# Optimization experiments

Hardware: AMD Instinct MI355X
Metric: run time of the kernel (lower is better)

Reference implementation:

```python
import jax, jax.numpy as jnp
import numpy as np

D, L, H = 256, 8, 64  # data_dim, latent_dim, hidden_dim (depth=3 hidden layers)


def setup_inputs() -> dict:
    key = jax.random.key(0)
    ks = jax.random.split(key, 9)
    s_in = 1.0 / np.sqrt(L)
    s_h = 1.0 / np.sqrt(H)
    return {
        "z": jax.random.normal(ks[0], (4096, D, L), dtype=jnp.float32),
        # stacked per-coordinate MLP params: layer i weight (D, in, out), bias (D, out)
        "W1": jax.random.uniform(ks[1], (D, L, H), jnp.float32, -s_in, s_in),
        "b1": jax.random.uniform(ks[2], (D, H), jnp.float32, -s_in, s_in),
        "W2": jax.random.uniform(ks[3], (D, H, H), jnp.float32, -s_h, s_h),
        "b2": jax.random.uniform(ks[4], (D, H), jnp.float32, -s_h, s_h),
        "W3": jax.random.uniform(ks[5], (D, H, H), jnp.float32, -s_h, s_h),
        "b3": jax.random.uniform(ks[6], (D, H), jnp.float32, -s_h, s_h),
        "Wo": jax.random.uniform(ks[7], (D, H, 1), jnp.float32, -s_h, s_h),
        "bo": jax.random.uniform(ks[8], (D, 1), jnp.float32, -s_h, s_h),
    }


def reference(z, W1, b1, W2, b2, W3, b3, Wo, bo):
    # Batched grouped MLP: all data_dim per-coordinate nets in one einsum per layer.
    h = jax.nn.silu(jnp.einsum("bdl,dlh->bdh", z, W1) + b1)   # (B, D, H)
    h = jax.nn.silu(jnp.einsum("bdh,dhk->bdk", h, W2) + b2)
    h = jax.nn.silu(jnp.einsum("bdh,dhk->bdk", h, W3) + b3)
    out = jnp.einsum("bdh,dho->bdo", h, Wo) + bo              # (B, D, 1)
    return out[..., 0]                                        # (B, D) == torch.cat(coords, dim=1)
```

## Files before the change

kernel.cpp:

```cpp
#include <hip/hip_runtime.h>
#include <hip/hip_bf16.h>


#define NDIM 256
#define LDIM 8
#define HDIM 64
#define BDIM 4096
#define BT   128

#define REC_W1P   0
#define REC_W2H   3072
#define REC_W2L   11264
#define REC_W3H   19456
#define REC_W3L   27648
#define REC_COEF  35840
#define REC_SIZE  36864

#define ACT_HI    0
#define OUTBUF    16384
#define LDS_SIZE  17408

typedef __bf16 bf16x8 __attribute__((ext_vector_type(8)));
typedef __bf16 bf16x4 __attribute__((ext_vector_type(4)));
typedef float  f32x4  __attribute__((ext_vector_type(4)));

__device__ __forceinline__ float silu_f(float x) {
  return x * __builtin_amdgcn_rcpf(1.0f + __expf(-x));
}

__global__ void setup_weights(const float* __restrict__ W1, const float* __restrict__ b1,
                              const float* __restrict__ W2, const float* __restrict__ b2,
                              const float* __restrict__ W3, const float* __restrict__ b3,
                              const float* __restrict__ Wo, char* __restrict__ ws) {
  const int d = blockIdx.x;
  const int y = blockIdx.y;
  const int t = threadIdx.x;
  __shared__ float tile[64 * 65];
  char* rec = ws + (size_t)d * REC_SIZE;

  if (y == 0) {
    for (int idx = t; idx < LDIM * HDIM; idx += 256)
      tile[(idx >> 6) * 65 + (idx & 63)] = W1[d * LDIM * HDIM + idx];
    __syncthreads();
    if (t < 64) {
      __bf16* w1p = (__bf16*)(rec + REC_W1P) + t * 24;
#pragma unroll
      for (int ks = 0; ks < 8; ++ks) {
        float f = tile[ks * 65 + t];
        __bf16 h = (__bf16)f;
        w1p[ks] = h;
        w1p[8 + ks] = h;
        w1p[16 + ks] = (__bf16)(f - (float)h);
      }
    }
    float* coef = (float*)(rec + REC_COEF);
    float v;
    if (t < 64)       v = b1[d * 64 + t];
    else if (t < 128) v = b2[d * 64 + (t - 64)];
    else if (t < 192) v = b3[d * 64 + (t - 128)];
    else              v = Wo[d * 64 + (t - 192)];
    coef[t] = v;
  } else {
    const float* src = (y == 1 ? W2 : W3) + (size_t)d * 4096;
    const int hibase = (y == 1 ? REC_W2H : REC_W3H);
    for (int idx = t; idx < 4096; idx += 256)
      tile[(idx >> 6) * 65 + (idx & 63)] = src[idx];
    __syncthreads();
    const int o = t >> 2;
    const int q = t & 3;
    bf16x8 h0, h1, l0, l1;
#pragma unroll
    for (int j = 0; j < 8; ++j) {
      float f = tile[(q * 16 + j) * 65 + o];
      __bf16 h = (__bf16)f;
      h0[j] = h; l0[j] = (__bf16)(f - (float)h);
      float g = tile[(q * 16 + 8 + j) * 65 + o];
      __bf16 hg = (__bf16)g;
      h1[j] = hg; l1[j] = (__bf16)(g - (float)hg);
    }
    char* dst = rec + hibase + o * 128 + q * 32;
    *(bf16x8*)(dst)              = h0;
    *(bf16x8*)(dst + 16)         = h1;
    *(bf16x8*)(dst + 8192)       = l0;
    *(bf16x8*)(dst + 8192 + 16)  = l1;
  }
}

__device__ __forceinline__ void mid_layer(const char* __restrict__ wh, const float* __restrict__ biasf,
                                          const char* __restrict__ smem, f32x4 (&acc)[2][4],
                                          int wm, int wp, int l15, int lg, int x7) {
  const int co = (lg ^ x7) * 16;
#pragma unroll
  for (int mt = 0; mt < 2; ++mt) {
    f32x4 b = *(const f32x4*)(biasf + wm * 32 + mt * 16 + lg * 4);
#pragma unroll
    for (int nt = 0; nt < 4; ++nt) acc[mt][nt] = b;
  }
  const char* aw[2];
  int ab[4];
#pragma unroll
  for (int mt = 0; mt < 2; ++mt) aw[mt] = wh + (wm * 32 + mt * 16 + l15) * 128 + lg * 16;
#pragma unroll
  for (int nt = 0; nt < 4; ++nt) ab[nt] = ACT_HI + (wp * 64 + nt * 16 + l15) * 128 + co;

#pragma unroll
  for (int ks = 0; ks < 2; ++ks) {
    const int kx = ks * 64;
    bf16x8 ah[2], al[2], bh[4];
#pragma unroll
    for (int mt = 0; mt < 2; ++mt) {
      const char* p = aw[mt] + kx;
      ah[mt] = *(const bf16x8*)p;
      al[mt] = *(const bf16x8*)(p + 8192);
    }
#pragma unroll
    for (int nt = 0; nt < 4; ++nt)
      bh[nt] = *(const bf16x8*)(smem + (ab[nt] ^ kx));
#pragma unroll
    for (int mt = 0; mt < 2; ++mt)
#pragma unroll
      for (int nt = 0; nt < 4; ++nt)
        acc[mt][nt] = __builtin_amdgcn_mfma_f32_16x16x32_bf16(ah[mt], bh[nt], acc[mt][nt], 0, 0, 0);
#pragma unroll
    for (int mt = 0; mt < 2; ++mt)
#pragma unroll
      for (int nt = 0; nt < 4; ++nt)
        acc[mt][nt] = __builtin_amdgcn_mfma_f32_16x16x32_bf16(al[mt], bh[nt], acc[mt][nt], 0, 0, 0);
  }
}

__device__ __forceinline__ void transition(f32x4 (&acc)[2][4], char* __restrict__ smem,
                                           int wm, int wp, int l15, int lg, int x7) {
  const int h8 = (lg & 1) * 8;
#pragma unroll
  for (int mt = 0; mt < 2; ++mt) {
    const int c = wm * 4 + mt * 2 + (lg >> 1);
    const int coff = ((c ^ x7) * 16) + h8;
#pragma unroll
    for (int nt = 0; nt < 4; ++nt) {
      const int r = wp * 64 + nt * 16 + l15;
      bf16x4 hv;
#pragma unroll
      for (int i = 0; i < 4; ++i)
        hv[i] = (__bf16)silu_f(acc[mt][nt][i]);
      *(bf16x4*)(smem + ACT_HI + r * 128 + coff) = hv;
    }
  }
}

__global__ __launch_bounds__(256, 3)
void mlp_main(const float* __restrict__ z, const char* __restrict__ ws,
              const float* __restrict__ bo, float* __restrict__ out) {
  __shared__ __align__(16) char smem[LDS_SIZE];

  const int bx  = (int)blockIdx.x;
  const int swz = (bx & 7) * 1024 + (bx >> 3);
  const int d   = swz >> 5;
  const int b0  = (swz & 31) * BT;

  const int t    = (int)threadIdx.x;
  const int lane = t & 63;
  const int wave = t >> 6;
  const int wm  = wave & 1;
  const int wp  = wave >> 1;
  const int l15 = lane & 15;
  const int lg  = lane >> 4;
  const int x7  = l15 & 7;

  const char* rec   = ws + (size_t)d * REC_SIZE;
  const float* coef = (const float*)(rec + REC_COEF);

  bf16x8 zf[4];
#pragma unroll
  for (int nt = 0; nt < 4; ++nt) {
    const int r = b0 + wp * 64 + nt * 16 + l15;
    const float* zp = z + ((size_t)r * NDIM + d) * LDIM;
    float4 q0 = *(const float4*)zp;
    float4 q1 = *(const float4*)(zp + 4);
    float f[8] = {q0.x, q0.y, q0.z, q0.w, q1.x, q1.y, q1.z, q1.w};
    bf16x8 hv, lv;
#pragma unroll
    for (int j = 0; j < 8; ++j) {
      __bf16 h = (__bf16)f[j];
      hv[j] = h;
      lv[j] = (__bf16)(f[j] - (float)h);
    }
    zf[nt] = (lg & 1) ? lv : hv;
  }

  f32x4 acc[2][4];

  {
    bf16x8 a1[2];
#pragma unroll
    for (int mt = 0; mt < 2; ++mt) {
      if (lg < 3) {
        a1[mt] = *(const bf16x8*)(rec + REC_W1P + (wm * 32 + mt * 16 + l15) * 48 + lg * 16);
      } else {
        a1[mt] = (bf16x8)((__bf16)0.0f);
      }
    }
#pragma unroll
    for (int mt = 0; mt < 2; ++mt) {
      f32x4 b = *(const f32x4*)(coef + wm * 32 + mt * 16 + lg * 4);
#pragma unroll
      for (int nt = 0; nt < 4; ++nt) acc[mt][nt] = b;
    }
#pragma unroll
    for (int mt = 0; mt < 2; ++mt)
#pragma unroll
      for (int nt = 0; nt < 4; ++nt)
        acc[mt][nt] = __builtin_amdgcn_mfma_f32_16x16x32_bf16(a1[mt], zf[nt], acc[mt][nt], 0, 0, 0);
  }

  transition(acc, smem, wm, wp, l15, lg, x7);
  __syncthreads();

  mid_layer(rec + REC_W2H, coef + 64, smem, acc, wm, wp, l15, lg, x7);
  __syncthreads();
  transition(acc, smem, wm, wp, l15, lg, x7);
  __syncthreads();

  mid_layer(rec + REC_W3H, coef + 128, smem, acc, wm, wp, l15, lg, x7);

  float* outBuf = (float*)(smem + OUTBUF);
  f32x4 wof[2];
#pragma unroll
  for (int mt = 0; mt < 2; ++mt)
    wof[mt] = *(const f32x4*)(coef + 192 + wm * 32 + mt * 16 + lg * 4);
#pragma unroll
  for (int nt = 0; nt < 4; ++nt) {
    float part = 0.0f;
#pragma unroll
    for (int mt = 0; mt < 2; ++mt)
#pragma unroll
      for (int i = 0; i < 4; ++i)
        part += silu_f(acc[mt][nt][i]) * wof[mt][i];
    part += __shfl_xor(part, 16);
    part += __shfl_xor(part, 32);
    if (lg == 0) outBuf[wm * 128 + wp * 64 + nt * 16 + l15] = part;
  }
  __syncthreads();
  if (t < BT) out[(size_t)(b0 + t) * NDIM + d] = outBuf[t] + outBuf[128 + t] + bo[d];
}

extern "C" void kernel_launch(void* const* d_in, const int* in_sizes, int n_in,
                              void* d_out, int out_size, void* d_ws, size_t ws_size,
                              hipStream_t stream) {
  const float* z  = (const float*)d_in[0];
  const float* W1 = (const float*)d_in[1];
  const float* b1 = (const float*)d_in[2];
  const float* W2 = (const float*)d_in[3];
  const float* b2 = (const float*)d_in[4];
  const float* W3 = (const float*)d_in[5];
  const float* b3 = (const float*)d_in[6];
  const float* Wo = (const float*)d_in[7];
  const float* bo = (const float*)d_in[8];
  float* out = (float*)d_out;
  char* ws = (char*)d_ws;

  setup_weights<<<dim3(NDIM, 3), 256, 0, stream>>>(W1, b1, W2, b2, W3, b3, Wo, ws);
  mlp_main<<<NDIM * (BDIM / BT), 256, 0, stream>>>(z, ws, bo, out);
}
```

Baseline: 198.4 us.

## Give each wave its own batch rows and all outputs to drop block barriers

Work is now split so each wave owns 32 batch rows and computes all 64 hidden outputs for them, rather than splitting the output dimension across wave pairs. Each wave keeps a private LDS activation slice, so every __syncthreads and the cross-wave output reduction buffer go away, and results are written straight to global memory. The occupancy hint rises from 3 to 4 blocks per SM. Each wave now loads the full weight fragments (twice as many A loads per MFMA), and the larger accumulator and weight register sets may add register pressure.

```diff
diff --git a/kernel.cpp b/kernel.cpp
--- a/kernel.cpp
+++ b/kernel.cpp
@@ -16,9 +16,7 @@
 #define REC_COEF  35840
 #define REC_SIZE  36864
 
-#define ACT_HI    0
-#define OUTBUF    16384
-#define LDS_SIZE  17408
+#define LDS_SIZE  16384
 
 typedef __bf16 bf16x8 __attribute__((ext_vector_type(8)));
 typedef __bf16 bf16x4 __attribute__((ext_vector_type(4)));
@@ -86,69 +84,7 @@
   }
 }
 
-__device__ __forceinline__ void mid_layer(const char* __restrict__ wh, const float* __restrict__ biasf,
-                                          const char* __restrict__ smem, f32x4 (&acc)[2][4],
-                                          int wm, int wp, int l15, int lg, int x7) {
-  const int co = (lg ^ x7) * 16;
-#pragma unroll
-  for (int mt = 0; mt < 2; ++mt) {
-    f32x4 b = *(const f32x4*)(biasf + wm * 32 + mt * 16 + lg * 4);
-#pragma unroll
-    for (int nt = 0; nt < 4; ++nt) acc[mt][nt] = b;
-  }
-  const char* aw[2];
-  int ab[4];
-#pragma unroll
-  for (int mt = 0; mt < 2; ++mt) aw[mt] = wh + (wm * 32 + mt * 16 + l15) * 128 + lg * 16;
-#pragma unroll
-  for (int nt = 0; nt < 4; ++nt) ab[nt] = ACT_HI + (wp * 64 + nt * 16 + l15) * 128 + co;
-
-#pragma unroll
-  for (int ks = 0; ks < 2; ++ks) {
-    const int kx = ks * 64;
-    bf16x8 ah[2], al[2], bh[4];
-#pragma unroll
-    for (int mt = 0; mt < 2; ++mt) {
-      const char* p = aw[mt] + kx;
-      ah[mt] = *(const bf16x8*)p;
-      al[mt] = *(const bf16x8*)(p + 8192);
-    }
-#pragma unroll
-    for (int nt = 0; nt < 4; ++nt)
-      bh[nt] = *(const bf16x8*)(smem + (ab[nt] ^ kx));
-#pragma unroll
-    for (int mt = 0; mt < 2; ++mt)
-#pragma unroll
-      for (int nt = 0; nt < 4; ++nt)
-        acc[mt][nt] = __builtin_amdgcn_mfma_f32_16x16x32_bf16(ah[mt], bh[nt], acc[mt][nt], 0, 0, 0);
-#pragma unroll
-    for (int mt = 0; mt < 2; ++mt)
-#pragma unroll
-      for (int nt = 0; nt < 4; ++nt)
-        acc[mt][nt] = __builtin_amdgcn_mfma_f32_16x16x32_bf16(al[mt], bh[nt], acc[mt][nt], 0, 0, 0);
-  }
-}
-
-__device__ __forceinline__ void transition(f32x4 (&acc)[2][4], char* __restrict__ smem,
-                                           int wm, int wp, int l15, int lg, int x7) {
-  const int h8 = (lg & 1) * 8;
-#pragma unroll
-  for (int mt = 0; mt < 2; ++mt) {
-    const int c = wm * 4 + mt * 2 + (lg >> 1);
-    const int coff = ((c ^ x7) * 16) + h8;
-#pragma unroll
-    for (int nt = 0; nt < 4; ++nt) {
-      const int r = wp * 64 + nt * 16 + l15;
-      bf16x4 hv;
-#pragma unroll
-      for (int i = 0; i < 4; ++i)
-        hv[i] = (__bf16)silu_f(acc[mt][nt][i]);
-      *(bf16x4*)(smem + ACT_HI + r * 128 + coff) = hv;
-    }
-  }
-}
-
-__global__ __launch_bounds__(256, 3)
+__global__ __launch_bounds__(256, 4)
 void mlp_main(const float* __restrict__ z, const char* __restrict__ ws,
               const float* __restrict__ bo, float* __restrict__ out) {
   __shared__ __align__(16) char smem[LDS_SIZE];
@@ -160,20 +96,21 @@
 
   const int t    = (int)threadIdx.x;
   const int lane = t & 63;
-  const int wave = t >> 6;
-  const int wm  = wave & 1;
-  const int wp  = wave >> 1;
-  const int l15 = lane & 15;
-  const int lg  = lane >> 4;
-  const int x7  = l15 & 7;
+  const int wq   = t >> 6;
+  const int l15  = lane & 15;
+  const int lg   = lane >> 4;
+  const int x7   = l15 & 7;
+  const int r0   = b0 + wq * 32;
+
+  char* act = smem + wq * 4096;
 
   const char* rec   = ws + (size_t)d * REC_SIZE;
   const float* coef = (const float*)(rec + REC_COEF);
 
-  bf16x8 zf[4];
-#pragma unroll
-  for (int nt = 0; nt < 4; ++nt) {
-    const int r = b0 + wp * 64 + nt * 16 + l15;
+  bf16x8 zf[2];
+#pragma unroll
+  for (int nt = 0; nt < 2; ++nt) {
+    const int r = r0 + nt * 16 + l15;
     const float* zp = z + ((size_t)r * NDIM + d) * LDIM;
     float4 q0 = *(const float4*)zp;
     float4 q1 = *(const float4*)(zp + 4);
@@ -188,60 +125,114 @@
     zf[nt] = (lg & 1) ? lv : hv;
   }
 
-  f32x4 acc[2][4];
+  f32x4 acc[4][2];
 
   {
-    bf16x8 a1[2];
-#pragma unroll
-    for (int mt = 0; mt < 2; ++mt) {
+    bf16x8 a1[4];
+#pragma unroll
+    for (int mt = 0; mt < 4; ++mt) {
       if (lg < 3) {
-        a1[mt] = *(const bf16x8*)(rec + REC_W1P + (wm * 32 + mt * 16 + l15) * 48 + lg * 16);
+        a1[mt] = *(const bf16x8*)(rec + REC_W1P + (mt * 16 + l15) * 48 + lg * 16);
       } else {
         a1[mt] = (bf16x8)((__bf16)0.0f);
       }
     }
 #pragma unroll
-    for (int mt = 0; mt < 2; ++mt) {
-      f32x4 b = *(const f32x4*)(coef + wm * 32 + mt * 16 + lg * 4);
-#pragma unroll
-      for (int nt = 0; nt < 4; ++nt) acc[mt][nt] = b;
-    }
-#pragma unroll
-    for (int mt = 0; mt < 2; ++mt)
-#pragma unroll
-      for (int nt = 0; nt < 4; ++nt)
+    for (int mt = 0; mt < 4; ++mt) {
+      f32x4 b = *(const f32x4*)(coef + mt * 16 + lg * 4);
+#pragma unroll
+      for (int nt = 0; nt < 2; ++nt) acc[mt][nt] = b;
+    }
+#pragma unroll
+    for (int mt = 0; mt < 4; ++mt)
+#pragma unroll
+      for (int nt = 0; nt < 2; ++nt)
         acc[mt][nt] = __builtin_amdgcn_mfma_f32_16x16x32_bf16(a1[mt], zf[nt], acc[mt][nt], 0, 0, 0);
   }
 
-  transition(acc, smem, wm, wp, l15, lg, x7);
-  __syncthreads();
-
-  mid_layer(rec + REC_W2H, coef + 64, smem, acc, wm, wp, l15, lg, x7);
-  __syncthreads();
-  transition(acc, smem, wm, wp, l15, lg, x7);
-  __syncthreads();
-
-  mid_layer(rec + REC_W3H, coef + 128, smem, acc, wm, wp, l15, lg, x7);
-
-  float* outBuf = (float*)(smem + OUTBUF);
-  f32x4 wof[2];
-#pragma unroll
-  for (int mt = 0; mt < 2; ++mt)
-    wof[mt] = *(const f32x4*)(coef + 192 + wm * 32 + mt * 16 + lg * 4);
-#pragma unroll
-  for (int nt = 0; nt < 4; ++nt) {
+#pragma unroll
+  for (int mt = 0; mt < 4; ++mt) {
+    const int cw = ((2 * mt + (lg >> 1)) ^ x7) * 16 + 8 * (lg & 1);
+#pragma unroll
+    for (int nt = 0; nt < 2; ++nt) {
+      const int rl = nt * 16 + l15;
+      bf16x4 hv;
+#pragma unroll
+      for (int i = 0; i < 4; ++i) hv[i] = (__bf16)silu_f(acc[mt][nt][i]);
+      *(bf16x4*)(act + rl * 128 + cw) = hv;
+    }
+  }
+
+#pragma unroll
+  for (int L = 0; L < 2; ++L) {
+    const char* wh = rec + (L == 0 ? REC_W2H : REC_W3H);
+    const float* biasf = coef + (L == 0 ? 64 : 128);
+#pragma unroll
+    for (int mt = 0; mt < 4; ++mt) {
+      f32x4 b = *(const f32x4*)(biasf + mt * 16 + lg * 4);
+#pragma unroll
+      for (int nt = 0; nt < 2; ++nt) acc[mt][nt] = b;
+    }
+#pragma unroll
+    for (int ks = 0; ks < 2; ++ks) {
+      bf16x8 ah[4], al[4], bh[2];
+#pragma unroll
+      for (int mt = 0; mt < 4; ++mt) {
+        const char* p = wh + (mt * 16 + l15) * 128 + ks * 64 + lg * 16;
+        ah[mt] = *(const bf16x8*)p;
+        al[mt] = *(const bf16x8*)(p + 8192);
+      }
+#pragma unroll
+      for (int nt = 0; nt < 2; ++nt) {
+        const int rl = nt * 16 + l15;
+        bh[nt] = *(const bf16x8*)(act + rl * 128 + (((4 * ks + lg) ^ x7) << 4));
+      }
+#pragma unroll
+      for (int mt = 0; mt < 4; ++mt)
+#pragma unroll
+        for (int nt = 0; nt < 2; ++nt)
+          acc[mt][nt] = __builtin_amdgcn_mfma_f32_16x16x32_bf16(ah[mt], bh[nt], acc[mt][nt], 0, 0, 0);
+#pragma unroll
+      for (int mt = 0; mt < 4; ++mt)
+#pragma unroll
+        for (int nt = 0; nt < 2; ++nt)
+          acc[mt][nt] = __builtin_amdgcn_mfma_f32_16x16x32_bf16(al[mt], bh[nt], acc[mt][nt], 0, 0, 0);
+    }
+
+    if (L == 0) {
+#pragma unroll
+      for (int mt = 0; mt < 4; ++mt) {
+        const int cw = ((2 * mt + (lg >> 1)) ^ x7) * 16 + 8 * (lg & 1);
+#pragma unroll
+        for (int nt = 0; nt < 2; ++nt) {
+          const int rl = nt * 16 + l15;
+          bf16x4 hv;
+#pragma unroll
+          for (int i = 0; i < 4; ++i) hv[i] = (__bf16)silu_f(acc[mt][nt][i]);
+          *(bf16x4*)(act + rl * 128 + cw) = hv;
+        }
+      }
+    }
+  }
+
+  f32x4 wof[4];
+#pragma unroll
+  for (int mt = 0; mt < 4; ++mt)
+    wof[mt] = *(const f32x4*)(coef + 192 + mt * 16 + lg * 4);
+  const float bov = bo[d];
+#pragma unroll
+  for (int nt = 0; nt < 2; ++nt) {
     float part = 0.0f;
 #pragma unroll
-    for (int mt = 0; mt < 2; ++mt)
+    for (int mt = 0; mt < 4; ++mt)
 #pragma unroll
       for (int i = 0; i < 4; ++i)
         part += silu_f(acc[mt][nt][i]) * wof[mt][i];
     part += __shfl_xor(part, 16);
     part += __shfl_xor(part, 32);
-    if (lg == 0) outBuf[wm * 128 + wp * 64 + nt * 16 + l15] = part;
-  }
-  __syncthreads();
-  if (t < BT) out[(size_t)(b0 + t) * NDIM + d] = outBuf[t] + outBuf[128 + t] + bo[d];
+    if (lg == 0)
+      out[(size_t)(r0 + nt * 16 + l15) * NDIM + d] = part + bov;
+  }
 }
 
 extern "C" void kernel_launch(void* const* d_in, const int* in_sizes, int n_in,
```

After: 238.7 us. 20.3% more time.
